# Kernel tuning notes

Hardware: AMD Instinct MI355X
Metric: run time of the kernel (lower is better)

Reference implementation:

```python
import jax, jax.numpy as jnp
import numpy as np

CLASS_NUM = 4            # number of positive classes
NUM_CLASSES = CLASS_NUM + 1  # last column is the negative class
W_P = 4.0
EPS = 1e-9
THR = 0.5


def setup_inputs() -> dict:
    key = jax.random.key(0)
    k1, k2 = jax.random.split(key)
    N = 4_000_000
    x = jax.random.normal(k1, (N, NUM_CLASSES), dtype=jnp.float32)
    t = jax.random.randint(k2, (N,), 0, NUM_CLASSES)
    return {"x": x, "t": t}


def _conf_mpu_loss(x, t):
    N = x.shape[0]
    p = jax.nn.softmax(x, axis=1)                       # [N, C]
    log_pneg = jnp.log(p[:, -1] + EPS)                  # [N]

    ones = jnp.ones((N,), dtype=jnp.float32)
    counts = jax.ops.segment_sum(ones, t, num_segments=NUM_CLASSES)  # per-class counts
    prior = counts[:CLASS_NUM] / N                      # empirical priors (positive classes)

    # loss_per_class: sum over samples with t==c of -log(p[n,c]+eps)
    logp_t = jnp.log(jnp.take_along_axis(p, t[:, None], axis=1)[:, 0] + EPS)
    class_losses = jax.ops.segment_sum(-logp_t, t, num_segments=NUM_CLASSES)

    # loss_per_class_neg: sum over samples with t==i (i positive) of -log(p_neg+eps)
    loss_neg = jax.ops.segment_sum(-log_pneg, t, num_segments=NUM_CLASSES)[:CLASS_NUM]

    # conf_loss_per_class
    conf = []
    for i in range(CLASS_NUM):
        mask = (p[:, i] > THR) & (t == i)
        nsel = jnp.sum(mask.astype(jnp.float32))
        li = jnp.sum(jnp.where(mask, -log_pneg / p[:, i], 0.0))
        conf.append(li / jnp.maximum(nsel, 1.0))        # li==0 when nsel==0
    mask_n = jnp.all(p <= THR, axis=1) & (t == CLASS_NUM)
    li_n = jnp.sum(jnp.where(mask_n, -log_pneg, 0.0))
    conf_neg = li_n / jnp.maximum(counts[CLASS_NUM], 1.0)  # li_n==0 when no selection
    conf_pos = jnp.stack(conf)                          # [CLASS_NUM]

    denom = jnp.maximum(1.0, counts[:CLASS_NUM])
    risk1 = jnp.sum(prior * class_losses[:CLASS_NUM] / denom)
    risk2 = jnp.sum(prior * conf_pos)
    risk3 = jnp.sum(prior * loss_neg / denom)
    risk4 = conf_neg

    positive_risk = W_P * (risk1 + risk2 - risk3)
    positive_risk = jnp.where(positive_risk < 0, 0.0, positive_risk)
    return positive_risk + risk4


def reference(x, t):
    return _conf_mpu_loss(x, t)
```

## Files before the change

kernel.cpp:

```cpp
#include <hip/hip_runtime.h>

namespace {
constexpr int BLOCK = 256;
constexpr int GRID = 2048;
constexpr int NACC = 22;
constexpr float WPF = 4.0f;
}

__device__ __forceinline__ float wave_reduce(float v) {
#pragma unroll
    for (int o = 32; o > 0; o >>= 1) v += __shfl_down(v, o, 64);
    return v;
}

__global__ __launch_bounds__(BLOCK) void mpu_main(const float* __restrict__ x,
                                                  const int* __restrict__ t,
                                                  float* __restrict__ acc, int N) {
    __shared__ float red[BLOCK / 64][NACC];

    float a[NACC];
#pragma unroll
    for (int j = 0; j < NACC; ++j) a[j] = 0.0f;

    auto process = [&](float x0, float x1, float x2, float x3, float x4, int tc) {
        const float mx = fmaxf(fmaxf(fmaxf(x0, x1), fmaxf(x2, x3)), x4);
        const float e0 = __expf(x0 - mx), e1 = __expf(x1 - mx),
                    e2 = __expf(x2 - mx), e3 = __expf(x3 - mx),
                    e4 = __expf(x4 - mx);
        const float sum = ((e0 + e1) + (e2 + e3)) + e4;
        const float base = mx + __logf(sum);
        const float nln = base - x4;
        const float xt = (tc == 0) ? x0 : (tc == 1) ? x1 : (tc == 2) ? x2
                       : (tc == 3) ? x3 : x4;
        const float et = (tc == 0) ? e0 : (tc == 1) ? e1 : (tc == 2) ? e2
                       : (tc == 3) ? e3 : e4;
        const float nlt = base - xt;

        const bool is0 = (tc == 0), is1 = (tc == 1), is2 = (tc == 2),
                   is3 = (tc == 3), is4 = (tc == 4);
        const bool sel = (et + et > sum);
        const bool alle = (sum >= 2.0f);
        const float confv = sel ? nln * sum * __builtin_amdgcn_rcpf(et) : 0.0f;
        const float confn = sel ? 1.0f : 0.0f;

        a[0] += is0 ? 1.0f : 0.0f;
        a[1] += is1 ? 1.0f : 0.0f;
        a[2] += is2 ? 1.0f : 0.0f;
        a[3] += is3 ? 1.0f : 0.0f;
        a[4] += is4 ? 1.0f : 0.0f;
        a[5] += is0 ? nlt : 0.0f;
        a[6] += is1 ? nlt : 0.0f;
        a[7] += is2 ? nlt : 0.0f;
        a[8] += is3 ? nlt : 0.0f;
        a[9]  += is0 ? nln : 0.0f;
        a[10] += is1 ? nln : 0.0f;
        a[11] += is2 ? nln : 0.0f;
        a[12] += is3 ? nln : 0.0f;
        a[13] += is0 ? confv : 0.0f;
        a[14] += is1 ? confv : 0.0f;
        a[15] += is2 ? confv : 0.0f;
        a[16] += is3 ? confv : 0.0f;
        a[17] += is0 ? confn : 0.0f;
        a[18] += is1 ? confn : 0.0f;
        a[19] += is2 ? confn : 0.0f;
        a[20] += is3 ? confn : 0.0f;
        a[21] += (is4 && alle) ? nln : 0.0f;
    };

    const int gid = blockIdx.x * BLOCK + threadIdx.x;
    const int stride = gridDim.x * BLOCK;
    const int nGroups = N >> 2;
    const float4* xv = reinterpret_cast<const float4*>(x);
    const int4* tv = reinterpret_cast<const int4*>(t);

    for (int g = gid; g < nGroups; g += stride) {
        const float4 v0 = xv[g * 5 + 0];
        const float4 v1 = xv[g * 5 + 1];
        const float4 v2 = xv[g * 5 + 2];
        const float4 v3 = xv[g * 5 + 3];
        const float4 v4 = xv[g * 5 + 4];
        const int4 tt = tv[g];
        process(v0.x, v0.y, v0.z, v0.w, v1.x, tt.x);
        process(v1.y, v1.z, v1.w, v2.x, v2.y, tt.y);
        process(v2.z, v2.w, v3.x, v3.y, v3.z, tt.z);
        process(v3.w, v4.x, v4.y, v4.z, v4.w, tt.w);
    }
    if (gid == 0) {
        for (int k = nGroups * 4; k < N; ++k)
            process(x[k * 5 + 0], x[k * 5 + 1], x[k * 5 + 2], x[k * 5 + 3],
                    x[k * 5 + 4], t[k]);
    }

    const int wave = threadIdx.x >> 6;
    const int lane = threadIdx.x & 63;
#pragma unroll
    for (int j = 0; j < NACC; ++j) {
        const float v = wave_reduce(a[j]);
        if (lane == 0) red[wave][j] = v;
    }
    __syncthreads();
    if (threadIdx.x < NACC) {
        const float v = red[0][threadIdx.x] + red[1][threadIdx.x] +
                        red[2][threadIdx.x] + red[3][threadIdx.x];
        atomicAdd(&acc[threadIdx.x], v);
    }
}

__global__ void mpu_final(const float* __restrict__ acc, float* __restrict__ out, int N) {
    if (threadIdx.x == 0 && blockIdx.x == 0) {
        const float invN = 1.0f / (float)N;
        float risk1 = 0.0f, risk2 = 0.0f, risk3 = 0.0f;
#pragma unroll
        for (int i = 0; i < 4; ++i) {
            const float cnt = acc[i];
            const float prior = cnt * invN;
            const float denom = fmaxf(1.0f, cnt);
            risk1 += prior * acc[5 + i] / denom;
            risk2 += prior * (acc[13 + i] / fmaxf(acc[17 + i], 1.0f));
            risk3 += prior * acc[9 + i] / denom;
        }
        const float risk4 = acc[21] / fmaxf(acc[4], 1.0f);
        float pos = WPF * (risk1 + risk2 - risk3);
        if (pos < 0.0f) pos = 0.0f;
        out[0] = pos + risk4;
    }
}

extern "C" void kernel_launch(void* const* d_in, const int* in_sizes, int n_in,
                              void* d_out, int out_size, void* d_ws, size_t ws_size,
                              hipStream_t stream) {
    const float* x = (const float*)d_in[0];
    const int* t = (const int*)d_in[1];
    float* out = (float*)d_out;
    float* acc = (float*)d_ws;
    const int N = in_sizes[1];

    hipMemsetAsync(acc, 0, NACC * sizeof(float), stream);

    const int nGroups = N >> 2;
    int grid = (nGroups + BLOCK - 1) / BLOCK;
    if (grid > GRID) grid = GRID;
    if (grid < 1) grid = 1;
    mpu_main<<<grid, BLOCK, 0, stream>>>(x, t, acc, N);
    mpu_final<<<1, 64, 0, stream>>>(acc, out, N);
}
```

Measured before the change: 148.8 us.

## Cut accumulators algebraically, count via wave ballots, one-shot 8-row-per-thread grid

The per-sample math is rewritten so risk1 and risk3 collapse into two positive-class sums, since prior/denom cancels to 1/N. Class and selection counts move from float accumulators to wave-wide ballot+popcount, and the negative count is derived as N minus the positive counts. The grid-stride loop becomes a single pass where each thread loads 8 rows at once, launching many more blocks. The goal is less register pressure, fewer reduction steps and more loads in flight, at the cost of more atomics from a larger grid.

After: 139.1 us. 1.07x faster.

```diff
diff --git a/kernel.cpp b/kernel.cpp
--- a/kernel.cpp
+++ b/kernel.cpp
@@ -2,9 +2,8 @@
 
 namespace {
 constexpr int BLOCK = 256;
-constexpr int GRID = 2048;
-constexpr int NACC = 22;
 constexpr float WPF = 4.0f;
+constexpr float LN2 = 0.69314718056f;
 }
 
 __device__ __forceinline__ float wave_reduce(float v) {
@@ -16,90 +15,88 @@
 __global__ __launch_bounds__(BLOCK) void mpu_main(const float* __restrict__ x,
                                                   const int* __restrict__ t,
                                                   float* __restrict__ acc, int N) {
-    __shared__ float red[BLOCK / 64][NACC];
+    __shared__ float red[BLOCK / 64][16];
 
-    float a[NACC];
-#pragma unroll
-    for (int j = 0; j < NACC; ++j) a[j] = 0.0f;
+    float S1 = 0.f, S3 = 0.f, li0 = 0.f, li1 = 0.f, li2 = 0.f, li3 = 0.f, liN = 0.f;
+    int c0 = 0, c1 = 0, c2 = 0, c3 = 0, n0 = 0, n1 = 0, n2 = 0, n3 = 0;
 
     auto process = [&](float x0, float x1, float x2, float x3, float x4, int tc) {
         const float mx = fmaxf(fmaxf(fmaxf(x0, x1), fmaxf(x2, x3)), x4);
-        const float e0 = __expf(x0 - mx), e1 = __expf(x1 - mx),
-                    e2 = __expf(x2 - mx), e3 = __expf(x3 - mx),
-                    e4 = __expf(x4 - mx);
+        const float e0 = __expf(x0 - mx), e1 = __expf(x1 - mx), e2 = __expf(x2 - mx),
+                    e3 = __expf(x3 - mx), e4 = __expf(x4 - mx);
         const float sum = ((e0 + e1) + (e2 + e3)) + e4;
-        const float base = mx + __logf(sum);
+        const float base = fmaf(__log2f(sum), LN2, mx);
         const float nln = base - x4;
         const float xt = (tc == 0) ? x0 : (tc == 1) ? x1 : (tc == 2) ? x2
                        : (tc == 3) ? x3 : x4;
-        const float et = (tc == 0) ? e0 : (tc == 1) ? e1 : (tc == 2) ? e2
-                       : (tc == 3) ? e3 : e4;
         const float nlt = base - xt;
+        const bool tpos = (tc < 4);
+        const bool sel = (nlt < LN2);
+        const bool alle = (sum >= 2.0f);
+        const float confv = sel ? nln * __expf(nlt) : 0.f;
 
-        const bool is0 = (tc == 0), is1 = (tc == 1), is2 = (tc == 2),
-                   is3 = (tc == 3), is4 = (tc == 4);
-        const bool sel = (et + et > sum);
-        const bool alle = (sum >= 2.0f);
-        const float confv = sel ? nln * sum * __builtin_amdgcn_rcpf(et) : 0.0f;
-        const float confn = sel ? 1.0f : 0.0f;
+        S1 += tpos ? nlt : 0.f;
+        S3 += tpos ? nln : 0.f;
+        li0 += (tc == 0) ? confv : 0.f;
+        li1 += (tc == 1) ? confv : 0.f;
+        li2 += (tc == 2) ? confv : 0.f;
+        li3 += (tc == 3) ? confv : 0.f;
+        liN += (!tpos && alle) ? nln : 0.f;
 
-        a[0] += is0 ? 1.0f : 0.0f;
-        a[1] += is1 ? 1.0f : 0.0f;
-        a[2] += is2 ? 1.0f : 0.0f;
-        a[3] += is3 ? 1.0f : 0.0f;
-        a[4] += is4 ? 1.0f : 0.0f;
-        a[5] += is0 ? nlt : 0.0f;
-        a[6] += is1 ? nlt : 0.0f;
-        a[7] += is2 ? nlt : 0.0f;
-        a[8] += is3 ? nlt : 0.0f;
-        a[9]  += is0 ? nln : 0.0f;
-        a[10] += is1 ? nln : 0.0f;
-        a[11] += is2 ? nln : 0.0f;
-        a[12] += is3 ? nln : 0.0f;
-        a[13] += is0 ? confv : 0.0f;
-        a[14] += is1 ? confv : 0.0f;
-        a[15] += is2 ? confv : 0.0f;
-        a[16] += is3 ? confv : 0.0f;
-        a[17] += is0 ? confn : 0.0f;
-        a[18] += is1 ? confn : 0.0f;
-        a[19] += is2 ? confn : 0.0f;
-        a[20] += is3 ? confn : 0.0f;
-        a[21] += (is4 && alle) ? nln : 0.0f;
+        const unsigned long long b0 = __ballot(tc == 0);
+        const unsigned long long b1 = __ballot(tc == 1);
+        const unsigned long long b2 = __ballot(tc == 2);
+        const unsigned long long b3 = __ballot(tc == 3);
+        const unsigned long long bs = __ballot(sel);
+        c0 += (int)__popcll(b0);
+        c1 += (int)__popcll(b1);
+        c2 += (int)__popcll(b2);
+        c3 += (int)__popcll(b3);
+        n0 += (int)__popcll(bs & b0);
+        n1 += (int)__popcll(bs & b1);
+        n2 += (int)__popcll(bs & b2);
+        n3 += (int)__popcll(bs & b3);
     };
 
-    const int gid = blockIdx.x * BLOCK + threadIdx.x;
-    const int stride = gridDim.x * BLOCK;
-    const int nGroups = N >> 2;
-    const float4* xv = reinterpret_cast<const float4*>(x);
-    const int4* tv = reinterpret_cast<const int4*>(t);
+    const int pid = blockIdx.x * BLOCK + threadIdx.x;
+    const int nOct = N >> 3;
 
-    for (int g = gid; g < nGroups; g += stride) {
-        const float4 v0 = xv[g * 5 + 0];
-        const float4 v1 = xv[g * 5 + 1];
-        const float4 v2 = xv[g * 5 + 2];
-        const float4 v3 = xv[g * 5 + 3];
-        const float4 v4 = xv[g * 5 + 4];
-        const int4 tt = tv[g];
-        process(v0.x, v0.y, v0.z, v0.w, v1.x, tt.x);
-        process(v1.y, v1.z, v1.w, v2.x, v2.y, tt.y);
-        process(v2.z, v2.w, v3.x, v3.y, v3.z, tt.z);
-        process(v3.w, v4.x, v4.y, v4.z, v4.w, tt.w);
+    if (pid < nOct) {
+        const float4* xv = reinterpret_cast<const float4*>(x) + (size_t)pid * 10;
+        const int4* tv = reinterpret_cast<const int4*>(t) + (size_t)pid * 2;
+        const float4 v0 = xv[0], v1 = xv[1], v2 = xv[2], v3 = xv[3], v4 = xv[4];
+        const float4 v5 = xv[5], v6 = xv[6], v7 = xv[7], v8 = xv[8], v9 = xv[9];
+        const int4 ta = tv[0], tb = tv[1];
+        process(v0.x, v0.y, v0.z, v0.w, v1.x, ta.x);
+        process(v1.y, v1.z, v1.w, v2.x, v2.y, ta.y);
+        process(v2.z, v2.w, v3.x, v3.y, v3.z, ta.z);
+        process(v3.w, v4.x, v4.y, v4.z, v4.w, ta.w);
+        process(v5.x, v5.y, v5.z, v5.w, v6.x, tb.x);
+        process(v6.y, v6.z, v6.w, v7.x, v7.y, tb.y);
+        process(v7.z, v7.w, v8.x, v8.y, v8.z, tb.z);
+        process(v8.w, v9.x, v9.y, v9.z, v9.w, tb.w);
     }
-    if (gid == 0) {
-        for (int k = nGroups * 4; k < N; ++k)
+    if (blockIdx.x == 0 && threadIdx.x == 0) {
+        for (int k = (N >> 3) << 3; k < N; ++k)
             process(x[k * 5 + 0], x[k * 5 + 1], x[k * 5 + 2], x[k * 5 + 3],
                     x[k * 5 + 4], t[k]);
     }
 
-    const int wave = threadIdx.x >> 6;
-    const int lane = threadIdx.x & 63;
+    const int wv = threadIdx.x >> 6, ln = threadIdx.x & 63;
+    float fr[7] = {S1, S3, li0, li1, li2, li3, liN};
 #pragma unroll
-    for (int j = 0; j < NACC; ++j) {
-        const float v = wave_reduce(a[j]);
-        if (lane == 0) red[wave][j] = v;
+    for (int j = 0; j < 7; ++j) {
+        const float v = wave_reduce(fr[j]);
+        if (ln == 0) red[wv][j] = v;
+    }
+    if (ln == 0) {
+        red[wv][7] = (float)c0;  red[wv][8] = (float)c1;
+        red[wv][9] = (float)c2;  red[wv][10] = (float)c3;
+        red[wv][11] = (float)n0; red[wv][12] = (float)n1;
+        red[wv][13] = (float)n2; red[wv][14] = (float)n3;
     }
     __syncthreads();
-    if (threadIdx.x < NACC) {
+    if (threadIdx.x < 15) {
         const float v = red[0][threadIdx.x] + red[1][threadIdx.x] +
                         red[2][threadIdx.x] + red[3][threadIdx.x];
         atomicAdd(&acc[threadIdx.x], v);
@@ -109,17 +106,14 @@
 __global__ void mpu_final(const float* __restrict__ acc, float* __restrict__ out, int N) {
     if (threadIdx.x == 0 && blockIdx.x == 0) {
         const float invN = 1.0f / (float)N;
-        float risk1 = 0.0f, risk2 = 0.0f, risk3 = 0.0f;
+        const float risk1 = acc[0] * invN;
+        const float risk3 = acc[1] * invN;
+        float risk2 = 0.0f;
 #pragma unroll
-        for (int i = 0; i < 4; ++i) {
-            const float cnt = acc[i];
-            const float prior = cnt * invN;
-            const float denom = fmaxf(1.0f, cnt);
-            risk1 += prior * acc[5 + i] / denom;
-            risk2 += prior * (acc[13 + i] / fmaxf(acc[17 + i], 1.0f));
-            risk3 += prior * acc[9 + i] / denom;
-        }
-        const float risk4 = acc[21] / fmaxf(acc[4], 1.0f);
+        for (int i = 0; i < 4; ++i)
+            risk2 += (acc[7 + i] * invN) * (acc[2 + i] / fmaxf(acc[11 + i], 1.0f));
+        const float c4 = (float)N - (acc[7] + acc[8] + acc[9] + acc[10]);
+        const float risk4 = acc[6] / fmaxf(c4, 1.0f);
         float pos = WPF * (risk1 + risk2 - risk3);
         if (pos < 0.0f) pos = 0.0f;
         out[0] = pos + risk4;
@@ -135,11 +129,10 @@
     float* acc = (float*)d_ws;
     const int N = in_sizes[1];
 
-    hipMemsetAsync(acc, 0, NACC * sizeof(float), stream);
+    hipMemsetAsync(acc, 0, 15 * sizeof(float), stream);
 
-    const int nGroups = N >> 2;
-    int grid = (nGroups + BLOCK - 1) / BLOCK;
-    if (grid > GRID) grid = GRID;
+    const int nOct = N >> 3;
+    int grid = (nOct + BLOCK - 1) / BLOCK;
     if (grid < 1) grid = 1;
     mpu_main<<<grid, BLOCK, 0, stream>>>(x, t, acc, N);
     mpu_final<<<1, 64, 0, stream>>>(acc, out, N);
```
